# Performance work log

Measured on AMD Instinct MI355X. Metric: run time of the kernel, lower is better.

The kernel has to match this reference:

```python
import jax, jax.numpy as jnp
import numpy as np

DIM = 512
HEADS = 8
WS = 8  # window_size


def setup_inputs() -> dict:
    key = jax.random.key(0)
    ks = jax.random.split(key, 7)
    b, c, h, w = 4, DIM, 192, 192
    x = jax.random.normal(ks[0], (b, c, h, w), dtype=jnp.float32)
    # conv1x1 weights are [out, in] matrices (kernel dim squeezed)
    wq = jax.random.normal(ks[1], (DIM, DIM), dtype=jnp.float32) * 0.02
    wk = jax.random.normal(ks[2], (DIM, DIM), dtype=jnp.float32) * 0.02
    wv = jax.random.normal(ks[3], (DIM, DIM), dtype=jnp.float32) * 0.02
    wo = jax.random.normal(ks[4], (DIM, DIM), dtype=jnp.float32) * 0.02
    bo = jax.random.normal(ks[5], (DIM,), dtype=jnp.float32) * 0.02
    # learned per-head additive bias over window tokens (trunc_normal std=0.02)
    beta = jax.random.normal(ks[6], (HEADS, WS * WS, WS * WS), dtype=jnp.float32) * 0.02
    return {"x": x, "wq": wq, "wk": wk, "wv": wv, "wo": wo, "bo": bo, "beta": beta}


def reference(x, wq, wk, wv, wo, bo, beta):
    b, c, h, w = x.shape
    s = WS
    pad_r = (-w) % s
    pad_b = (-h) % s
    x = jnp.pad(x, ((0, 0), (0, 0), (0, pad_b), (0, pad_r)))
    H, W = h + pad_b, w + pad_r
    nh, nw = H // s, W // s
    n = s * s
    head_dim = c // HEADS
    scale = head_dim ** -0.5
    # window partition: (b, c, nh, s, nw, s) -> (b*nh*nw, c, n)
    xw = x.reshape(b, c, nh, s, nw, s).transpose(0, 2, 4, 1, 3, 5).reshape(b * nh * nw, c, n)
    B = xw.shape[0]
    q = jnp.einsum('oc,bcn->bon', wq, xw).reshape(B, HEADS, head_dim, n)
    k = jnp.einsum('oc,bcn->bon', wk, xw).reshape(B, HEADS, head_dim, n)
    v = jnp.einsum('oc,bcn->bon', wv, xw).reshape(B, HEADS, head_dim, n)
    attn = jnp.einsum('bhdn,bhdm->bhnm', q, k) * scale + beta  # [B,H,n,n]
    attn = jax.nn.softmax(attn, axis=-1)
    o = jnp.einsum('bhnm,bhdm->bhdn', attn, v).reshape(B, c, n)
    o = jnp.einsum('oc,bcn->bon', wo, o) + bo[None, :, None]
    # window merge back to image
    out = o.reshape(b, nh, nw, c, s, s).transpose(0, 3, 1, 4, 2, 5).reshape(b, c, H, W)
    return out[:, :, :h, :w]
```

## Files before the change

### kernel.cpp

```cpp
#include <hip/hip_runtime.h>

typedef unsigned short ushort_t;
typedef __attribute__((ext_vector_type(4))) float f32x4;
typedef __attribute__((ext_vector_type(8))) short short8;

__device__ __forceinline__ ushort_t f2bf(float f) {
  union { float f; unsigned u; } v; v.f = f;
  unsigned r = v.u + 0x7fffu + ((v.u >> 16) & 1u);
  return (ushort_t)(r >> 16);
}
__device__ __forceinline__ unsigned pack2(float lo, float hi) {
  return (unsigned)f2bf(lo) | ((unsigned)f2bf(hi) << 16);
}

#define WLOAD(dst, p) \
  asm volatile("global_load_dwordx4 %0, %1, off" : "=v"(dst) : "v"((unsigned long long)(p)))
#define VMWD(n, S) asm volatile("s_waitcnt vmcnt(" #n ")" \
    : "+v"(ws[S][0]), "+v"(ws[S][1]), "+v"(ws[S][2]))

__global__ __launch_bounds__(256) void prep_k(const float* __restrict__ x,
                                              const float* __restrict__ wq,
                                              const float* __restrict__ wk,
                                              const float* __restrict__ wv,
                                              const float* __restrict__ wo,
                                              ushort_t* __restrict__ wB,
                                              ushort_t* __restrict__ xT) {
  __shared__ ushort_t tile[128 * 80];
  int bid = blockIdx.x;
  int tid = threadIdx.x;
  if (bid < 1024) {
    int idx = (bid * 256 + tid) * 4;
    int m = idx >> 18;
    int off = idx & 0x3ffff;
    const float* s = (m == 0) ? wq : (m == 1) ? wk : (m == 2) ? wv : wo;
    float4 v = *(const float4*)(s + off);
    ushort4 o;
    o.x = f2bf(v.x); o.y = f2bf(v.y); o.z = f2bf(v.z); o.w = f2bf(v.w);
    *(ushort4*)(wB + idx) = o;
    return;
  }
  int xb_id = bid - 1024;
  int win = xb_id >> 2, kc = xb_id & 3;
  int b = win / 576, rem = win % 576, wh = rem / 24, ww = rem % 24;
  {
    int c_l = tid >> 1, half = tid & 1;
    const float* xb = x + ((((size_t)b * 512 + kc * 128 + c_l) * 192 + wh * 8) * 192 + ww * 8);
#pragma unroll
    for (int ii = 0; ii < 4; ++ii) {
      int i = half * 4 + ii;
      float4 v0 = *(const float4*)(xb + i * 192);
      float4 v1 = *(const float4*)(xb + i * 192 + 4);
      uint4 u;
      u.x = (unsigned)f2bf(v0.x) | ((unsigned)f2bf(v0.y) << 16);
      u.y = (unsigned)f2bf(v0.z) | ((unsigned)f2bf(v0.w) << 16);
      u.z = (unsigned)f2bf(v1.x) | ((unsigned)f2bf(v1.y) << 16);
      u.w = (unsigned)f2bf(v1.z) | ((unsigned)f2bf(v1.w) << 16);
      *(uint4*)&tile[c_l * 80 + i * 8] = u;
    }
  }
  __syncthreads();
  {
    int tok = tid >> 2, q = tid & 3;
    unsigned w[16];
#pragma unroll
    for (int k = 0; k < 16; ++k) {
      unsigned lo = tile[(q * 32 + 2 * k) * 80 + tok];
      unsigned hi = tile[(q * 32 + 2 * k + 1) * 80 + tok];
      w[k] = lo | (hi << 16);
    }
    ushort_t* d = xT + ((size_t)(win * 64 + tok) * 512 + kc * 128 + q * 32);
#pragma unroll
    for (int s2 = 0; s2 < 4; ++s2) {
      uint4 u; u.x = w[s2 * 4 + 0]; u.y = w[s2 * 4 + 1]; u.z = w[s2 * 4 + 2]; u.w = w[s2 * 4 + 3];
      *(uint4*)(d + s2 * 8) = u;
    }
  }
}

__global__ __launch_bounds__(512, 1) void qkv_attn10_k(const ushort_t* __restrict__ xT,
                                                       const ushort_t* __restrict__ wB,
                                                       const float* __restrict__ beta,
                                                       ushort_t* __restrict__ O) {
  __shared__ ushort_t xws[64 * 520];
  __shared__ ushort_t qs[2][64 * 72];
  __shared__ ushort_t ks[2][64 * 72];
  __shared__ ushort_t vs[2][64 * 72];
  int win = blockIdx.x;
  int t0 = win * 64;
  int tid = threadIdx.x, lane = tid & 63, wid = tid >> 6;
  int l15 = lane & 15, l4 = lane >> 4;

  {
    int token = tid >> 3, cb = (tid & 7) * 64;
    const uint4* src = (const uint4*)(xT + (size_t)(t0 + token) * 512 + cb);
    uint4* dst = (uint4*)&xws[token * 520 + cb];
#pragma unroll
    for (int s2 = 0; s2 < 8; ++s2) dst[s2] = src[s2];
  }
  __syncthreads();

  const f32x4 z = {0.f, 0.f, 0.f, 0.f};

  const ushort_t* wbase[4];
#pragma unroll
  for (int hc = 0; hc < 4; ++hc)
    wbase[hc] = wB + (size_t)(hc * 128 + wid * 16 + l15) * 512 + l4 * 8;

  short8 ws[4][3];

#define ISSUE(S, HC, KN) do {                                              \
    const ushort_t* _p = wbase[HC] + (KN) * 32;                            \
    WLOAD(ws[S][0], _p);                                                   \
    WLOAD(ws[S][1], _p + 262144);                                          \
    WLOAD(ws[S][2], _p + 524288);                                          \
  } while (0)

#pragma unroll
  for (int hcc = 0; hcc < 4; ++hcc) {
    f32x4 aq[4], ak[4], av[4];
#pragma unroll
    for (int i = 0; i < 4; ++i) { aq[i] = z; ak[i] = z; av[i] = z; }

    ISSUE(0, hcc, 0); ISSUE(1, hcc, 1); ISSUE(2, hcc, 2); ISSUE(3, hcc, 3);

#pragma unroll
    for (int kk = 0; kk < 16; ++kk) {
      const int s = kk & 3;
      if (kk <= 12) { VMWD(9, s); }
      else if (kk == 13) { VMWD(6, s); }
      else if (kk == 14) { VMWD(3, s); }
      else { VMWD(0, s); }
#pragma unroll
      for (int nt = 0; nt < 4; ++nt) {
        short8 a = *(const short8*)&xws[(nt * 16 + l15) * 520 + kk * 32 + l4 * 8];
        aq[nt] = __builtin_amdgcn_mfma_f32_16x16x32_bf16(a, ws[s][0], aq[nt], 0, 0, 0);
        ak[nt] = __builtin_amdgcn_mfma_f32_16x16x32_bf16(a, ws[s][1], ak[nt], 0, 0, 0);
        av[nt] = __builtin_amdgcn_mfma_f32_16x16x32_bf16(a, ws[s][2], av[nt], 0, 0, 0);
      }
      if (kk + 4 < 16) ISSUE(s, hcc, kk + 4);
    }

    int hw = wid >> 2;
    int dd = (wid * 16 + l15) & 63;
#pragma unroll
    for (int nt = 0; nt < 4; ++nt) {
#pragma unroll
      for (int r = 0; r < 4; ++r) {
        int n = nt * 16 + l4 * 4 + r;
        qs[hw][n * 72 + dd] = f2bf(aq[nt][r]);
        ks[hw][n * 72 + dd] = f2bf(ak[nt][r]);
      }
      uint2 u;
      u.x = pack2(av[nt][0], av[nt][1]);
      u.y = pack2(av[nt][2], av[nt][3]);
      *(uint2*)&vs[hw][dd * 72 + nt * 16 + l4 * 4] = u;
    }
    __syncthreads();

    int hh = wid >> 2, rowg = wid & 3;
    int h = hcc * 2 + hh;
    f32x4 sA[4];
#pragma unroll
    for (int i = 0; i < 4; ++i) sA[i] = z;
#pragma unroll
    for (int kk = 0; kk < 2; ++kk) {
      short8 aF = *(const short8*)&qs[hh][(rowg * 16 + l15) * 72 + kk * 32 + l4 * 8];
#pragma unroll
      for (int mt = 0; mt < 4; ++mt) {
        short8 bF = *(const short8*)&ks[hh][(mt * 16 + l15) * 72 + kk * 32 + l4 * 8];
        sA[mt] = __builtin_amdgcn_mfma_f32_16x16x32_bf16(aF, bF, sA[mt], 0, 0, 0);
      }
    }
    const float* betah = beta + h * 4096;
    float p[4][4];
    float rmax[4] = {-1e30f, -1e30f, -1e30f, -1e30f};
#pragma unroll
    for (int mt = 0; mt < 4; ++mt)
#pragma unroll
      for (int r = 0; r < 4; ++r) {
        int n = rowg * 16 + l4 * 4 + r;
        float val = sA[mt][r] * 0.125f + betah[n * 64 + mt * 16 + l15];
        p[mt][r] = val;
        rmax[r] = fmaxf(rmax[r], val);
      }
#pragma unroll
    for (int m = 1; m <= 8; m <<= 1)
#pragma unroll
      for (int r = 0; r < 4; ++r) rmax[r] = fmaxf(rmax[r], __shfl_xor(rmax[r], m, 64));
    float rsum[4] = {0.f, 0.f, 0.f, 0.f};
#pragma unroll
    for (int mt = 0; mt < 4; ++mt)
#pragma unroll
      for (int r = 0; r < 4; ++r) {
        p[mt][r] = __expf(p[mt][r] - rmax[r]);
        rsum[r] += p[mt][r];
      }
#pragma unroll
    for (int m = 1; m <= 8; m <<= 1)
#pragma unroll
      for (int r = 0; r < 4; ++r) rsum[r] += __shfl_xor(rsum[r], m, 64);
    float rinv[4];
#pragma unroll
    for (int r = 0; r < 4; ++r) rinv[r] = 1.f / rsum[r];
#pragma unroll
    for (int mt = 0; mt < 4; ++mt)
#pragma unroll
      for (int r = 0; r < 4; ++r)
        qs[hh][(rowg * 16 + l4 * 4 + r) * 72 + mt * 16 + l15] = f2bf(p[mt][r] * rinv[r]);

    f32x4 oA[4];
#pragma unroll
    for (int i = 0; i < 4; ++i) oA[i] = z;
#pragma unroll
    for (int kk = 0; kk < 2; ++kk) {
      short8 aF = *(const short8*)&qs[hh][(rowg * 16 + l15) * 72 + kk * 32 + l4 * 8];
#pragma unroll
      for (int dt = 0; dt < 4; ++dt) {
        short8 bF = *(const short8*)&vs[hh][(dt * 16 + l15) * 72 + kk * 32 + l4 * 8];
        oA[dt] = __builtin_amdgcn_mfma_f32_16x16x32_bf16(aF, bF, oA[dt], 0, 0, 0);
      }
    }
#pragma unroll
    for (int dt = 0; dt < 4; ++dt)
#pragma unroll
      for (int r = 0; r < 4; ++r) {
        int n = rowg * 16 + l4 * 4 + r;
        O[(size_t)(t0 + n) * 512 + h * 64 + dt * 16 + l15] = f2bf(oA[dt][r]);
      }
    __syncthreads();
  }
#undef ISSUE
}

__global__ __launch_bounds__(256) void proj_kb(const ushort_t* __restrict__ O,
                                               const ushort_t* __restrict__ woB,
                                               const float* __restrict__ bo,
                                               float* __restrict__ out) {
  __shared__ ushort_t ows[64 * 136];
  int bid = blockIdx.x;
  int wg = (bid & 7) * 576 + (bid >> 3);
  int win = wg >> 1, mo = (wg & 1) * 256;
  int b = win / 576, rem = win % 576, wh = rem / 24, ww = rem % 24;
  int tid = threadIdx.x, lane = tid & 63, wid = tid >> 6;
  int l15 = lane & 15, l4 = lane >> 4;
  int t0 = win * 64;
  f32x4 z = {0.f, 0.f, 0.f, 0.f};
  f32x4 acc[4][4];
#pragma unroll
  for (int i = 0; i < 4; ++i)
#pragma unroll
    for (int j = 0; j < 4; ++j) acc[i][j] = z;
  int stok = tid >> 2, sq = tid & 3;
  for (int kcc = 0; kcc < 4; ++kcc) {
    {
      const uint4* src = (const uint4*)(O + ((size_t)(t0 + stok) * 512 + kcc * 128 + sq * 32));
      uint4* dstv = (uint4*)&ows[stok * 136 + sq * 32];
#pragma unroll
      for (int s2 = 0; s2 < 4; ++s2) dstv[s2] = src[s2];
    }
    __syncthreads();
#pragma unroll
    for (int kk = 0; kk < 4; ++kk) {
      short8 bF[4];
#pragma unroll
      for (int nt = 0; nt < 4; ++nt)
        bF[nt] = *(const short8*)&ows[(nt * 16 + l15) * 136 + kk * 32 + l4 * 8];
      int cg = kcc * 128 + kk * 32 + l4 * 8;
#pragma unroll
      for (int mt = 0; mt < 4; ++mt) {
        int orow = mo + wid * 64 + mt * 16 + l15;
        short8 aF = *(const short8*)(woB + (size_t)orow * 512 + cg);
#pragma unroll
        for (int nt = 0; nt < 4; ++nt)
          acc[mt][nt] = __builtin_amdgcn_mfma_f32_16x16x32_bf16(aF, bF[nt], acc[mt][nt], 0, 0, 0);
      }
    }
    __syncthreads();
  }
#pragma unroll
  for (int mt = 0; mt < 4; ++mt) {
#pragma unroll
    for (int r = 0; r < 4; ++r) {
      int o = mo + wid * 64 + mt * 16 + l4 * 4 + r;
      float bias = bo[o];
#pragma unroll
      for (int nt = 0; nt < 4; ++nt) {
        int tok = nt * 16 + l15;
        int i = tok >> 3, j = tok & 7;
        out[(((size_t)b * 512 + o) * 192 + wh * 8 + i) * 192 + ww * 8 + j] = acc[mt][nt][r] + bias;
      }
    }
  }
}

extern "C" void kernel_launch(void* const* d_in, const int* in_sizes, int n_in,
                              void* d_out, int out_size, void* d_ws, size_t ws_size,
                              hipStream_t stream) {
  const float* x    = (const float*)d_in[0];
  const float* wq   = (const float*)d_in[1];
  const float* wk   = (const float*)d_in[2];
  const float* wv   = (const float*)d_in[3];
  const float* wo   = (const float*)d_in[4];
  const float* bo   = (const float*)d_in[5];
  const float* beta = (const float*)d_in[6];

  ushort_t* wB = (ushort_t*)d_ws;
  ushort_t* xT = (ushort_t*)((char*)d_ws + (size_t)2097152);
  ushort_t* O  = (ushort_t*)((char*)d_ws + (size_t)2097152 + (size_t)147456 * 1024);

  prep_k<<<10240, 256, 0, stream>>>(x, wq, wk, wv, wo, wB, xT);
  qkv_attn10_k<<<2304, 512, 0, stream>>>(xT, wB, beta, O);
  proj_kb<<<4608, 256, 0, stream>>>(O, wB + 3 * 262144, bo, (float*)d_out);
}
```

Before: 906.0 us.

## Fuse output projection into window attention kernel, dropping intermediate O buffer

```diff
diff --git a/kernel.cpp b/kernel.cpp
--- a/kernel.cpp
+++ b/kernel.cpp
@@ -12,11 +12,6 @@
 __device__ __forceinline__ unsigned pack2(float lo, float hi) {
   return (unsigned)f2bf(lo) | ((unsigned)f2bf(hi) << 16);
 }
-
-#define WLOAD(dst, p) \
-  asm volatile("global_load_dwordx4 %0, %1, off" : "=v"(dst) : "v"((unsigned long long)(p)))
-#define VMWD(n, S) asm volatile("s_waitcnt vmcnt(" #n ")" \
-    : "+v"(ws[S][0]), "+v"(ws[S][1]), "+v"(ws[S][2]))
 
 __global__ __launch_bounds__(256) void prep_k(const float* __restrict__ x,
                                               const float* __restrict__ wq,
@@ -77,15 +72,19 @@
   }
 }
 
-__global__ __launch_bounds__(512, 1) void qkv_attn10_k(const ushort_t* __restrict__ xT,
-                                                       const ushort_t* __restrict__ wB,
-                                                       const float* __restrict__ beta,
-                                                       ushort_t* __restrict__ O) {
+__global__ __launch_bounds__(512, 1) void fused_k(const ushort_t* __restrict__ xT,
+                                                  const ushort_t* __restrict__ wB,
+                                                  const float* __restrict__ beta,
+                                                  const float* __restrict__ bo,
+                                                  float* __restrict__ out) {
   __shared__ ushort_t xws[64 * 520];
   __shared__ ushort_t qs[2][64 * 72];
   __shared__ ushort_t ks[2][64 * 72];
   __shared__ ushort_t vs[2][64 * 72];
-  int win = blockIdx.x;
+  __shared__ ushort_t obuf[64 * 264];
+  int bid = blockIdx.x;
+  int win = (bid & 7) * 288 + (bid >> 3);
+  int b = win / 576, rem = win % 576, wh = rem / 24, ww = rem % 24;
   int t0 = win * 64;
   int tid = threadIdx.x, lane = tid & 63, wid = tid >> 6;
   int l15 = lane & 15, l4 = lane >> 4;
@@ -100,46 +99,35 @@
   __syncthreads();
 
   const f32x4 z = {0.f, 0.f, 0.f, 0.f};
-
-  const ushort_t* wbase[4];
-#pragma unroll
-  for (int hc = 0; hc < 4; ++hc)
-    wbase[hc] = wB + (size_t)(hc * 128 + wid * 16 + l15) * 512 + l4 * 8;
-
-  short8 ws[4][3];
-
-#define ISSUE(S, HC, KN) do {                                              \
-    const ushort_t* _p = wbase[HC] + (KN) * 32;                            \
-    WLOAD(ws[S][0], _p);                                                   \
-    WLOAD(ws[S][1], _p + 262144);                                          \
-    WLOAD(ws[S][2], _p + 524288);                                          \
-  } while (0)
-
-#pragma unroll
+  const ushort_t* woB = wB + 3 * 262144;
+
+  f32x4 pacc[4][4];
+#pragma unroll
+  for (int i = 0; i < 4; ++i)
+#pragma unroll
+    for (int j = 0; j < 4; ++j) pacc[i][j] = z;
+
   for (int hcc = 0; hcc < 4; ++hcc) {
     f32x4 aq[4], ak[4], av[4];
 #pragma unroll
     for (int i = 0; i < 4; ++i) { aq[i] = z; ak[i] = z; av[i] = z; }
-
-    ISSUE(0, hcc, 0); ISSUE(1, hcc, 1); ISSUE(2, hcc, 2); ISSUE(3, hcc, 3);
-
+    int ocol = hcc * 128 + wid * 16 + l15;
+    const ushort_t* wqr = wB + (size_t)ocol * 512 + l4 * 8;
+    const ushort_t* wkr = wqr + 262144;
+    const ushort_t* wvr = wqr + 524288;
 #pragma unroll
     for (int kk = 0; kk < 16; ++kk) {
-      const int s = kk & 3;
-      if (kk <= 12) { VMWD(9, s); }
-      else if (kk == 13) { VMWD(6, s); }
-      else if (kk == 14) { VMWD(3, s); }
-      else { VMWD(0, s); }
+      short8 bq = *(const short8*)(wqr + kk * 32);
+      short8 bk = *(const short8*)(wkr + kk * 32);
+      short8 bv = *(const short8*)(wvr + kk * 32);
 #pragma unroll
       for (int nt = 0; nt < 4; ++nt) {
         short8 a = *(const short8*)&xws[(nt * 16 + l15) * 520 + kk * 32 + l4 * 8];
-        aq[nt] = __builtin_amdgcn_mfma_f32_16x16x32_bf16(a, ws[s][0], aq[nt], 0, 0, 0);
-        ak[nt] = __builtin_amdgcn_mfma_f32_16x16x32_bf16(a, ws[s][1], ak[nt], 0, 0, 0);
-        av[nt] = __builtin_amdgcn_mfma_f32_16x16x32_bf16(a, ws[s][2], av[nt], 0, 0, 0);
-      }
-      if (kk + 4 < 16) ISSUE(s, hcc, kk + 4);
-    }
-
+        aq[nt] = __builtin_amdgcn_mfma_f32_16x16x32_bf16(a, bq, aq[nt], 0, 0, 0);
+        ak[nt] = __builtin_amdgcn_mfma_f32_16x16x32_bf16(a, bk, ak[nt], 0, 0, 0);
+        av[nt] = __builtin_amdgcn_mfma_f32_16x16x32_bf16(a, bv, av[nt], 0, 0, 0);
+      }
+    }
     int hw = wid >> 2;
     int dd = (wid * 16 + l15) & 63;
 #pragma unroll
@@ -221,73 +209,51 @@
       }
     }
 #pragma unroll
-    for (int dt = 0; dt < 4; ++dt)
+    for (int dt = 0; dt < 4; ++dt) {
+      int col = (hcc & 1) * 128 + hh * 64 + dt * 16 + l15;
 #pragma unroll
       for (int r = 0; r < 4; ++r) {
         int n = rowg * 16 + l4 * 4 + r;
-        O[(size_t)(t0 + n) * 512 + h * 64 + dt * 16 + l15] = f2bf(oA[dt][r]);
-      }
+        obuf[n * 264 + col] = f2bf(oA[dt][r]);
+      }
+    }
     __syncthreads();
-  }
-#undef ISSUE
-}
-
-__global__ __launch_bounds__(256) void proj_kb(const ushort_t* __restrict__ O,
-                                               const ushort_t* __restrict__ woB,
-                                               const float* __restrict__ bo,
-                                               float* __restrict__ out) {
-  __shared__ ushort_t ows[64 * 136];
-  int bid = blockIdx.x;
-  int wg = (bid & 7) * 576 + (bid >> 3);
-  int win = wg >> 1, mo = (wg & 1) * 256;
-  int b = win / 576, rem = win % 576, wh = rem / 24, ww = rem % 24;
-  int tid = threadIdx.x, lane = tid & 63, wid = tid >> 6;
-  int l15 = lane & 15, l4 = lane >> 4;
-  int t0 = win * 64;
-  f32x4 z = {0.f, 0.f, 0.f, 0.f};
-  f32x4 acc[4][4];
-#pragma unroll
-  for (int i = 0; i < 4; ++i)
-#pragma unroll
-    for (int j = 0; j < 4; ++j) acc[i][j] = z;
-  int stok = tid >> 2, sq = tid & 3;
-  for (int kcc = 0; kcc < 4; ++kcc) {
-    {
-      const uint4* src = (const uint4*)(O + ((size_t)(t0 + stok) * 512 + kcc * 128 + sq * 32));
-      uint4* dstv = (uint4*)&ows[stok * 136 + sq * 32];
-#pragma unroll
-      for (int s2 = 0; s2 < 4; ++s2) dstv[s2] = src[s2];
-    }
-    __syncthreads();
-#pragma unroll
-    for (int kk = 0; kk < 4; ++kk) {
-      short8 bF[4];
-#pragma unroll
-      for (int nt = 0; nt < 4; ++nt)
-        bF[nt] = *(const short8*)&ows[(nt * 16 + l15) * 136 + kk * 32 + l4 * 8];
-      int cg = kcc * 128 + kk * 32 + l4 * 8;
-#pragma unroll
-      for (int mt = 0; mt < 4; ++mt) {
-        int orow = mo + wid * 64 + mt * 16 + l15;
-        short8 aF = *(const short8*)(woB + (size_t)orow * 512 + cg);
-#pragma unroll
-        for (int nt = 0; nt < 4; ++nt)
-          acc[mt][nt] = __builtin_amdgcn_mfma_f32_16x16x32_bf16(aF, bF[nt], acc[mt][nt], 0, 0, 0);
-      }
-    }
-    __syncthreads();
-  }
+
+    if (hcc & 1) {
+      int pp = hcc >> 1;
+#pragma unroll
+      for (int kcc = 0; kcc < 2; ++kcc) {
+#pragma unroll
+        for (int kk = 0; kk < 4; ++kk) {
+          int cg = kcc * 128 + kk * 32 + l4 * 8;
+          short8 bF[4];
+#pragma unroll
+          for (int nt = 0; nt < 4; ++nt)
+            bF[nt] = *(const short8*)&obuf[(nt * 16 + l15) * 264 + cg];
+#pragma unroll
+          for (int mt = 0; mt < 4; ++mt) {
+            int orow = wid * 64 + mt * 16 + l15;
+            short8 aF = *(const short8*)(woB + (size_t)orow * 512 + pp * 256 + cg);
+#pragma unroll
+            for (int nt = 0; nt < 4; ++nt)
+              pacc[mt][nt] = __builtin_amdgcn_mfma_f32_16x16x32_bf16(aF, bF[nt], pacc[mt][nt], 0, 0, 0);
+          }
+        }
+      }
+    }
+  }
+
 #pragma unroll
   for (int mt = 0; mt < 4; ++mt) {
 #pragma unroll
     for (int r = 0; r < 4; ++r) {
-      int o = mo + wid * 64 + mt * 16 + l4 * 4 + r;
+      int o = wid * 64 + mt * 16 + l4 * 4 + r;
       float bias = bo[o];
 #pragma unroll
       for (int nt = 0; nt < 4; ++nt) {
         int tok = nt * 16 + l15;
         int i = tok >> 3, j = tok & 7;
-        out[(((size_t)b * 512 + o) * 192 + wh * 8 + i) * 192 + ww * 8 + j] = acc[mt][nt][r] + bias;
+        out[(((size_t)b * 512 + o) * 192 + wh * 8 + i) * 192 + ww * 8 + j] = pacc[mt][nt][r] + bias;
       }
     }
   }
@@ -306,9 +272,7 @@
 
   ushort_t* wB = (ushort_t*)d_ws;
   ushort_t* xT = (ushort_t*)((char*)d_ws + (size_t)2097152);
-  ushort_t* O  = (ushort_t*)((char*)d_ws + (size_t)2097152 + (size_t)147456 * 1024);
 
   prep_k<<<10240, 256, 0, stream>>>(x, wq, wk, wv, wo, wB, xT);
-  qkv_attn10_k<<<2304, 512, 0, stream>>>(xT, wB, beta, O);
-  proj_kb<<<4608, 256, 0, stream>>>(O, wB + 3 * 262144, bo, (float*)d_out);
-}
+  fused_k<<<2304, 512, 0, stream>>>(xT, wB, beta, bo, (float*)d_out);
+}
```

After: 907.3 us. About the same (+0.1%).
